# Kernel optimization log

Hardware: AMD Instinct MI355X
Metric: run time of the kernel (lower is better)

## Reference

```python
import jax, jax.numpy as jnp
import numpy as np
import math

N, T, V, C = 64, 256, 25, 64  # batch, frames, joints, channels (in==out)
D = C  # out_channels
EPS = 1e-5


def _shift_indices(v, c):
    i = np.arange(v)[:, None]
    j = np.arange(c)[None, :]
    shift_in = ((i * c + j + j * c) % (c * v)).reshape(-1)
    shift_out = ((i * c + j - j * c) % (c * v)).reshape(-1)
    return shift_in.astype(np.int64), shift_out.astype(np.int64)


def setup_inputs() -> dict:
    key = jax.random.key(0)
    k1, k2 = jax.random.split(key)
    si, so = _shift_indices(V, D)
    return {
        "x0": jax.random.normal(k1, (N, T, V, C), dtype=jnp.float32),
        "Linear_weight": jax.random.normal(k2, (C, D), dtype=jnp.float32) * math.sqrt(1.0 / D),
        "Linear_bias": jnp.zeros((1, 1, D), dtype=jnp.float32),
        "Feature_Mask": jnp.zeros((1, V, C), dtype=jnp.float32),
        "gamma": jnp.ones((V * D,), dtype=jnp.float32),
        "beta": jnp.zeros((V * D,), dtype=jnp.float32),
        "shift_in": jnp.asarray(si),
        "shift_out": jnp.asarray(so),
    }


def reference(x0, Linear_weight, Linear_bias, Feature_Mask, gamma, beta, shift_in, shift_out):
    n, t, v, c = x0.shape
    d = Linear_weight.shape[1]
    # shift-in gather over flattened (node, channel) axis
    x = x0.reshape(n * t, v * c)[:, shift_in].reshape(n * t, v, c)
    # learned feature mask (tanh + 1)
    x = x * (jnp.tanh(Feature_Mask) + 1.0)
    # pointwise channel transform + bias
    x = jnp.einsum('nwc,cd->nwd', x, Linear_weight) + Linear_bias
    # shift-out gather
    x = x.reshape(n * t, v * d)[:, shift_out]
    # BatchNorm1d (training mode): batch stats over n*t rows, biased var
    mean = jnp.mean(x, axis=0)
    var = jnp.var(x, axis=0)
    x = (x - mean) * (gamma / jnp.sqrt(var + EPS)) + beta
    # residual (in_channels == out_channels -> identity down) + ReLU
    y = jax.nn.relu(x.reshape(n, t, v, d) + x0)
    # original returns (n, out_channels, t, v)
    return jnp.transpose(y, (0, 3, 1, 2))
```

## Files before the change

### kernel.cpp

```cpp
#include <hip/hip_runtime.h>
#include <math.h>


typedef __attribute__((ext_vector_type(8))) short bf16x8;
typedef __attribute__((ext_vector_type(4))) float f32x4;

__device__ __forceinline__ ushort f2bf(float f) {
  uint u; __builtin_memcpy(&u, &f, 4);
  u += 0x7fffu + ((u >> 16) & 1u);
  return (ushort)(u >> 16);
}
__device__ __forceinline__ float bf2f(ushort b) {
  uint u = ((uint)b) << 16; float f; __builtin_memcpy(&f, &u, 4); return f;
}

__global__ void k_prep(const float* __restrict__ mask, float* __restrict__ ws) {
  int i = blockIdx.x * 256 + threadIdx.x;
  if (i < 1600) {
    int w = i >> 6, c = i & 63;
    int wr = (w + c) % 25;
    ((ushort*)ws)[wr * 64 + c] = f2bf(tanhf(mask[i]) + 1.0f);
  }
  for (int j = 8000 + i; j < 8000 + 64 * 3200; j += gridDim.x * 256)
    ws[j] = 0.0f;
}

__global__ void k_finalize(const float* __restrict__ gamma,
                           const float* __restrict__ beta,
                           float* __restrict__ ws) {
  int q = blockIdx.x * 256 + threadIdx.x;
  if (q >= 1600) return;
  float sum = 0.f, sq = 0.f;
  #pragma unroll 4
  for (int s = 0; s < 64; ++s) {
    sum += ws[8000 + s * 3200 + q];
    sq  += ws[8000 + s * 3200 + 1600 + q];
  }
  const float inv = 1.0f / 16384.0f;
  float mean = sum * inv;
  float var  = sq * inv - mean * mean;
  float istd = rsqrtf(var + 1e-5f);
  int w = q >> 6, d = q & 63;
  int p = ((w + d) % 25) * 64 + d;
  float mul = gamma[p] * istd;
  ws[4800 + q] = mul;
  ws[6400 + q] = beta[p] - mean * mul;
}

template<int PASS>
__launch_bounds__(256, 4)
__global__ void k_main(const float* __restrict__ x0,
                       const float* __restrict__ Wg,
                       float* ws,
                       float* __restrict__ out) {
  __shared__ __align__(8)  ushort s_maskm[1600];
  __shared__ __align__(16) ushort s_A[4096];
  __shared__ float s_raw[PASS == 2 ? 3400 : 4];
  __shared__ float s_aux[3200];

  const int tid = threadIdx.x;
  const int lr  = tid & 63;
  const int wid = tid >> 6;

  for (int i = tid; i < 800; i += 256)
    ((uint*)s_maskm)[i] = ((const uint*)ws)[i];
  for (int i = tid; i < 2048; i += 256)
    ((uint*)s_A)[i] = 0u;

  bf16x8 wfrag[2][4];
  #pragma unroll
  for (int ks = 0; ks < 2; ++ks)
    #pragma unroll
    for (int nt = 0; nt < 4; ++nt) {
      const int d = nt * 16 + (lr & 15);
      const int cb = ks * 32 + (lr >> 4) * 8;
      #pragma unroll
      for (int j = 0; j < 8; ++j)
        wfrag[ks][nt][j] = (short)f2bf(Wg[(cb + j) * 64 + d]);
    }

  float cmul[16], cadd[16];
  float ssum[16], ssq[16];
  #pragma unroll
  for (int k = 0; k < 16; ++k) { ssum[k] = 0.f; ssq[k] = 0.f; }
  if constexpr (PASS == 2) {
    #pragma unroll
    for (int nt = 0; nt < 4; ++nt)
      #pragma unroll
      for (int r = 0; r < 4; ++r) {
        int row = wid * 16 + (lr >> 4) * 4 + r;
        int w = row & 31;
        int d = nt * 16 + (lr & 15);
        int qq = (w < 25) ? (w * 64 + d) : 0;
        cmul[nt * 4 + r] = ws[4800 + qq];
        cadd[nt * 4 + r] = ws[6400 + qq];
      }
  }

  const int row_base = blockIdx.x * 16;
  const int n  = row_base >> 8;
  const int t0 = row_base & 255;

  if constexpr (PASS == 1) {
    for (int i = tid; i < 3200; i += 256) s_aux[i] = 0.f;
  }
  __syncthreads();

  float4 cur0, cur1, cur2, cur3, nxt0, nxt1, nxt2, nxt3;
  {
    const float4* p = (const float4*)(x0 + (size_t)row_base * 1600);
    cur0 = p[tid]; cur1 = p[tid + 256]; cur2 = p[tid + 512];
    if (tid < 32) cur3 = p[tid + 768];
  }

  for (int rp = 0; rp < 16; rp += 2) {
    #pragma unroll
    for (int s = 0; s < 4; ++s) {
      if (s == 3 && tid >= 32) break;
      int i4 = (s < 3) ? (tid + s * 256) : (768 + tid);
      float4 v = (s == 0) ? cur0 : (s == 1) ? cur1 : (s == 2) ? cur2 : cur3;
      int r2 = (i4 >= 400) ? 1 : 0;
      int p4 = (i4 - r2 * 400) * 4;
      int wr = p4 >> 6, c0 = p4 & 63;
      if constexpr (PASS == 2)
        *(float4*)&s_raw[r2 * 1700 + wr * 68 + c0] = v;
      uint2 mm = *(const uint2*)&s_maskm[p4];
      float va[4] = {v.x, v.y, v.z, v.w};
      float ma[4] = {bf2f((ushort)(mm.x & 0xffff)), bf2f((ushort)(mm.x >> 16)),
                     bf2f((ushort)(mm.y & 0xffff)), bf2f((ushort)(mm.y >> 16))};
      int wbase = wr + 100 - c0;
      #pragma unroll
      for (int j = 0; j < 4; ++j) {
        int w = (wbase - j) % 25;
        int row = r2 * 32 + w;
        int byte = (row * 128 + (c0 + j) * 2) ^ ((w & 7) << 4);
        *(ushort*)((char*)s_A + byte) = f2bf(va[j] * ma[j]);
      }
    }

    if (rp + 2 < 16) {
      const float4* p = (const float4*)(x0 + (size_t)(row_base + rp + 2) * 1600);
      nxt0 = p[tid]; nxt1 = p[tid + 256]; nxt2 = p[tid + 512];
      if (tid < 32) nxt3 = p[tid + 768];
    }
    __syncthreads();

    const int arow = wid * 16 + (lr & 15);
    bf16x8 afrag[2];
    #pragma unroll
    for (int ks = 0; ks < 2; ++ks) {
      int byte = (arow * 128 + ks * 64 + (lr >> 4) * 16) ^ ((arow & 7) << 4);
      afrag[ks] = *(const bf16x8*)((const char*)s_A + byte);
    }
    f32x4 acc[4];
    #pragma unroll
    for (int nt = 0; nt < 4; ++nt) {
      acc[nt] = (f32x4){0.f, 0.f, 0.f, 0.f};
      #pragma unroll
      for (int ks = 0; ks < 2; ++ks)
        acc[nt] = __builtin_amdgcn_mfma_f32_16x16x32_bf16(afrag[ks], wfrag[ks][nt], acc[nt], 0, 0, 0);
    }

    if constexpr (PASS == 1) {
      #pragma unroll
      for (int nt = 0; nt < 4; ++nt)
        #pragma unroll
        for (int r = 0; r < 4; ++r) {
          float y = acc[nt][r];
          ssum[nt * 4 + r] += y;
          ssq [nt * 4 + r]  = fmaf(y, y, ssq[nt * 4 + r]);
        }
      __syncthreads();
    } else {
      #pragma unroll
      for (int nt = 0; nt < 4; ++nt)
        #pragma unroll
        for (int r = 0; r < 4; ++r) {
          int row = wid * 16 + (lr >> 4) * 4 + r;
          int r2 = row >> 5;
          int w  = row & 31;
          if (w < 25) {
            int d  = nt * 16 + (lr & 15);
            int wp = (w + d) % 25;
            float y = fmaf(acc[nt][r], cmul[nt * 4 + r], cadd[nt * 4 + r]);
            y += s_raw[r2 * 1700 + wp * 68 + d];
            s_aux[d * 50 + r2 * 25 + wp] = fmaxf(y, 0.f);
          }
        }
      __syncthreads();
      const size_t obase = (size_t)n * 409600 + (size_t)(t0 + rp) * 25;
      for (int i = tid; i < 3200; i += 256) {
        int d   = i / 50;
        int rem = i - d * 50;
        int r2  = rem / 25;
        int wp  = rem - r2 * 25;
        out[obase + (size_t)d * 6400 + r2 * 25 + wp] = s_aux[i];
      }
      __syncthreads();
    }

    if (rp + 2 < 16) {
      cur0 = nxt0; cur1 = nxt1; cur2 = nxt2;
      if (tid < 32) cur3 = nxt3;
    }
  }

  if constexpr (PASS == 1) {
    #pragma unroll
    for (int nt = 0; nt < 4; ++nt)
      #pragma unroll
      for (int r = 0; r < 4; ++r) {
        int row = wid * 16 + (lr >> 4) * 4 + r;
        int w = row & 31;
        if (w < 25) {
          int q = w * 64 + nt * 16 + (lr & 15);
          atomicAdd(&s_aux[q],        ssum[nt * 4 + r]);
          atomicAdd(&s_aux[1600 + q], ssq [nt * 4 + r]);
        }
      }
    __syncthreads();
    float* rep = ws + 8000 + (blockIdx.x & 63) * 3200;
    for (int i = tid; i < 3200; i += 256)
      atomicAdd(&rep[i], s_aux[i]);
  }
}

extern "C" void kernel_launch(void* const* d_in, const int* in_sizes, int n_in,
                              void* d_out, int out_size, void* d_ws, size_t ws_size,
                              hipStream_t stream) {
  const float* x0    = (const float*)d_in[0];
  const float* W     = (const float*)d_in[1];
  const float* mask  = (const float*)d_in[3];
  const float* gamma = (const float*)d_in[4];
  const float* beta  = (const float*)d_in[5];
  float* ws  = (float*)d_ws;
  float* out = (float*)d_out;

  k_prep    <<<200,  256, 0, stream>>>(mask, ws);
  k_main<1> <<<1024, 256, 0, stream>>>(x0, W, ws, out);
  k_finalize<<<7,    256, 0, stream>>>(gamma, beta, ws);
  k_main<2> <<<1024, 256, 0, stream>>>(x0, W, ws, out);
}
```

Before: 368.5 us.

## Materialize GEMM output to workspace and split epilogue into separate transpose kernel

When the workspace is large enough, a new path runs the mask-scaled GEMM once and writes the un-normalized outputs to the workspace. It stores per-block partial statistics in slots, reduces them in a separate kernel, then a tiled epilogue kernel reads y and x0 back to apply BN, the residual and ReLU, and writes the transposed output with float4 stores. This avoids recomputing the GEMM in a second pass and the scalar strided output stores, but adds an extra write and read of a 100MB intermediate. The fallback path also loses its register prefetch of the next x0 rows.

```diff
diff --git a/kernel.cpp b/kernel.cpp
--- a/kernel.cpp
+++ b/kernel.cpp
@@ -14,7 +14,213 @@
   uint u = ((uint)b) << 16; float f; __builtin_memcpy(&f, &u, 4); return f;
 }
 
-__global__ void k_prep(const float* __restrict__ mask, float* __restrict__ ws) {
+#define YOFF    0u
+#define SLOTOFF 26214400u
+#define SUMOFF  32768000u
+#define PRMOFF  32771200u
+#define WS_NEED ((size_t)(32771200u + 3200u) * 4u)
+
+__global__ __launch_bounds__(256, 5)
+void k_gemm(const float* __restrict__ x0, const float* __restrict__ Wg,
+            const float* __restrict__ FM, float* __restrict__ ws) {
+  __shared__ ushort s_maskm[1600];
+  __shared__ float  s_u[3200];
+  ushort* s_A = (ushort*)s_u;
+
+  const int tid = threadIdx.x;
+  const int lr  = tid & 63;
+  const int wid = tid >> 6;
+
+  for (int i = tid; i < 1600; i += 256) {
+    int w = i >> 6, c = i & 63;
+    int wr = (w + c) % 25;
+    s_maskm[wr * 64 + c] = f2bf(tanhf(FM[i]) + 1.0f);
+  }
+  for (int i = tid; i < 2048; i += 256) ((uint*)s_A)[i] = 0u;
+
+  bf16x8 wfrag[2][4];
+  #pragma unroll
+  for (int ks = 0; ks < 2; ++ks)
+    #pragma unroll
+    for (int nt = 0; nt < 4; ++nt) {
+      const int d = nt * 16 + (lr & 15);
+      const int cb = ks * 32 + (lr >> 4) * 8;
+      #pragma unroll
+      for (int j = 0; j < 8; ++j)
+        wfrag[ks][nt][j] = (short)f2bf(Wg[(cb + j) * 64 + d]);
+    }
+
+  float ssum[16], ssq[16];
+  #pragma unroll
+  for (int k = 0; k < 16; ++k) { ssum[k] = 0.f; ssq[k] = 0.f; }
+
+  const int row_base = blockIdx.x * 8;
+  __syncthreads();
+
+  for (int rp = 0; rp < 8; rp += 2) {
+    const float* xrow = x0 + (size_t)(row_base + rp) * 1600;
+    for (int i4 = tid; i4 < 800; i4 += 256) {
+      float4 v = ((const float4*)xrow)[i4];
+      int r2 = (i4 >= 400) ? 1 : 0;
+      int p4 = (i4 - r2 * 400) * 4;
+      int wr = p4 >> 6, c0 = p4 & 63;
+      uint2 mm = *(const uint2*)&s_maskm[p4];
+      float va[4] = {v.x, v.y, v.z, v.w};
+      float ma[4] = {bf2f((ushort)(mm.x & 0xffff)), bf2f((ushort)(mm.x >> 16)),
+                     bf2f((ushort)(mm.y & 0xffff)), bf2f((ushort)(mm.y >> 16))};
+      int w = (wr + 100 - c0) % 25;
+      #pragma unroll
+      for (int j = 0; j < 4; ++j) {
+        int row = r2 * 32 + w;
+        int byte = (row * 128 + (c0 + j) * 2) ^ ((w & 7) << 4);
+        *(ushort*)((char*)s_A + byte) = f2bf(va[j] * ma[j]);
+        w = (w == 0) ? 24 : (w - 1);
+      }
+    }
+    __syncthreads();
+
+    const int arow = wid * 16 + (lr & 15);
+    bf16x8 afrag[2];
+    #pragma unroll
+    for (int ks = 0; ks < 2; ++ks) {
+      int byte = (arow * 128 + ks * 64 + (lr >> 4) * 16) ^ ((arow & 7) << 4);
+      afrag[ks] = *(const bf16x8*)((const char*)s_A + byte);
+    }
+    f32x4 acc[4];
+    #pragma unroll
+    for (int nt = 0; nt < 4; ++nt) {
+      acc[nt] = (f32x4){0.f, 0.f, 0.f, 0.f};
+      #pragma unroll
+      for (int ks = 0; ks < 2; ++ks)
+        acc[nt] = __builtin_amdgcn_mfma_f32_16x16x32_bf16(afrag[ks], wfrag[ks][nt], acc[nt], 0, 0, 0);
+    }
+
+    #pragma unroll
+    for (int nt = 0; nt < 4; ++nt)
+      #pragma unroll
+      for (int r = 0; r < 4; ++r) {
+        float y = acc[nt][r];
+        ssum[nt * 4 + r] += y;
+        ssq [nt * 4 + r]  = fmaf(y, y, ssq[nt * 4 + r]);
+        int mrow = wid * 16 + (lr >> 4) * 4 + r;
+        int r2 = mrow >> 5, w = mrow & 31;
+        if (w < 25)
+          ws[YOFF + (size_t)(row_base + rp + r2) * 1600 + w * 64 + nt * 16 + (lr & 15)] = y;
+      }
+    __syncthreads();
+  }
+
+  #pragma unroll
+  for (int nt = 0; nt < 4; ++nt)
+    #pragma unroll
+    for (int r = 0; r < 4; ++r) {
+      int mrow = wid * 16 + (lr >> 4) * 4 + r;
+      int w = mrow & 31;
+      if (mrow < 32 && w < 25) {
+        int q = w * 64 + nt * 16 + (lr & 15);
+        s_u[q]        = ssum[nt * 4 + r];
+        s_u[1600 + q] = ssq [nt * 4 + r];
+      }
+    }
+  __syncthreads();
+  #pragma unroll
+  for (int nt = 0; nt < 4; ++nt)
+    #pragma unroll
+    for (int r = 0; r < 4; ++r) {
+      int mrow = wid * 16 + (lr >> 4) * 4 + r;
+      int w = mrow & 31;
+      if (mrow >= 32 && w < 25) {
+        int q = w * 64 + nt * 16 + (lr & 15);
+        s_u[q]        += ssum[nt * 4 + r];
+        s_u[1600 + q] += ssq [nt * 4 + r];
+      }
+    }
+  __syncthreads();
+  for (int i = tid; i < 3200; i += 256)
+    ws[SLOTOFF + (size_t)blockIdx.x * 3200 + i] = s_u[i];
+}
+
+__global__ void k_reduce(float* __restrict__ ws) {
+  int gid = blockIdx.x * 256 + threadIdx.x;
+  int q  = gid % 3200;
+  int sc = gid / 3200;
+  size_t base = SLOTOFF + (size_t)sc * 256 * 3200 + q;
+  float s = 0.f;
+  #pragma unroll 8
+  for (int k = 0; k < 256; ++k)
+    s += ws[base + (size_t)k * 3200];
+  atomicAdd(&ws[SUMOFF + q], s);
+}
+
+__global__ void k_params(const float* __restrict__ gamma,
+                         const float* __restrict__ beta,
+                         float* __restrict__ ws) {
+  int p = blockIdx.x * 256 + threadIdx.x;
+  if (p >= 1600) return;
+  int u = p >> 6, d = p & 63;
+  int w = (u + 75 - d) % 25;
+  int q = w * 64 + d;
+  const float inv = 1.0f / 16384.0f;
+  float mean = ws[SUMOFF + q] * inv;
+  float var  = ws[SUMOFF + 1600 + q] * inv - mean * mean;
+  float istd = rsqrtf(var + 1e-5f);
+  float mul = gamma[p] * istd;
+  ws[PRMOFF + p]        = mul;
+  ws[PRMOFF + 1600 + p] = beta[p] - mean * mul;
+}
+
+__global__ __launch_bounds__(256, 2)
+void k_epi(const float* __restrict__ x0, const float* __restrict__ ws,
+           float* __restrict__ out) {
+  __shared__ float yt[16 * 25 * 17];
+  __shared__ float xt[16 * 25 * 17];
+  __shared__ float pm[2][25 * 17];
+
+  const int tid = threadIdx.x;
+  const int n  = blockIdx.x >> 4;
+  const int t0 = (blockIdx.x & 15) * 16;
+  const size_t base_in = ((size_t)n * 256 + t0) * 1600;
+  const size_t base_out = (size_t)n * 409600 + (size_t)t0 * 25;
+
+  for (int dq = 0; dq < 4; ++dq) {
+    const int dbase = dq * 16;
+    for (int i4 = tid; i4 < 1600; i4 += 256) {
+      int t = i4 / 100, rem = i4 % 100;
+      int w = rem >> 2, f4 = rem & 3;
+      size_t g = base_in + (size_t)t * 1600 + w * 64 + dbase + f4 * 4;
+      float4 vy = *(const float4*)&ws[YOFF + g];
+      float4 vx = *(const float4*)&x0[g];
+      *(float4*)&yt[(t * 25 + w) * 17 + f4 * 4] = vy;
+      *(float4*)&xt[(t * 25 + w) * 17 + f4 * 4] = vx;
+    }
+    for (int i = tid; i < 400; i += 256) {
+      int u = i >> 4, dd = i & 15;
+      pm[0][u * 17 + dd] = ws[PRMOFF + u * 64 + dbase + dd];
+      pm[1][u * 17 + dd] = ws[PRMOFF + 1600 + u * 64 + dbase + dd];
+    }
+    __syncthreads();
+
+    for (int i4 = tid; i4 < 1600; i4 += 256) {
+      int dl = i4 / 100;
+      int d  = dbase + dl;
+      int p4 = (i4 % 100) * 4;
+      float4 o;
+      #pragma unroll
+      for (int e = 0; e < 4; ++e) {
+        int p = p4 + e;
+        int t = p / 25, u = p - t * 25;
+        int w = (u + 75 - d) % 25;
+        float val = fmaf(yt[(t * 25 + w) * 17 + dl], pm[0][u * 17 + dl],
+                         pm[1][u * 17 + dl]) + xt[(t * 25 + u) * 17 + dl];
+        o[e] = fmaxf(val, 0.f);
+      }
+      *(float4*)&out[base_out + (size_t)d * 6400 + p4] = o;
+    }
+    __syncthreads();
+  }
+}
+
+__global__ void k_prep_f(const float* __restrict__ mask, float* __restrict__ ws) {
   int i = blockIdx.x * 256 + threadIdx.x;
   if (i < 1600) {
     int w = i >> 6, c = i & 63;
@@ -25,9 +231,9 @@
     ws[j] = 0.0f;
 }
 
-__global__ void k_finalize(const float* __restrict__ gamma,
-                           const float* __restrict__ beta,
-                           float* __restrict__ ws) {
+__global__ void k_finalize_f(const float* __restrict__ gamma,
+                             const float* __restrict__ beta,
+                             float* __restrict__ ws) {
   int q = blockIdx.x * 256 + threadIdx.x;
   if (q >= 1600) return;
   float sum = 0.f, sq = 0.f;
@@ -49,10 +255,10 @@
 
 template<int PASS>
 __launch_bounds__(256, 4)
-__global__ void k_main(const float* __restrict__ x0,
-                       const float* __restrict__ Wg,
-                       float* ws,
-                       float* __restrict__ out) {
+__global__ void k_main_f(const float* __restrict__ x0,
+                         const float* __restrict__ Wg,
+                         float* ws,
+                         float* __restrict__ out) {
   __shared__ __align__(8)  ushort s_maskm[1600];
   __shared__ __align__(16) ushort s_A[4096];
   __shared__ float s_raw[PASS == 2 ? 3400 : 4];
@@ -106,19 +312,10 @@
   }
   __syncthreads();
 
-  float4 cur0, cur1, cur2, cur3, nxt0, nxt1, nxt2, nxt3;
-  {
-    const float4* p = (const float4*)(x0 + (size_t)row_base * 1600);
-    cur0 = p[tid]; cur1 = p[tid + 256]; cur2 = p[tid + 512];
-    if (tid < 32) cur3 = p[tid + 768];
-  }
-
   for (int rp = 0; rp < 16; rp += 2) {
-    #pragma unroll
-    for (int s = 0; s < 4; ++s) {
-      if (s == 3 && tid >= 32) break;
-      int i4 = (s < 3) ? (tid + s * 256) : (768 + tid);
-      float4 v = (s == 0) ? cur0 : (s == 1) ? cur1 : (s == 2) ? cur2 : cur3;
+    const float* xrow = x0 + (size_t)(row_base + rp) * 1600;
+    for (int i4 = tid; i4 < 800; i4 += 256) {
+      float4 v = ((const float4*)xrow)[i4];
       int r2 = (i4 >= 400) ? 1 : 0;
       int p4 = (i4 - r2 * 400) * 4;
       int wr = p4 >> 6, c0 = p4 & 63;
@@ -136,12 +333,6 @@
         int byte = (row * 128 + (c0 + j) * 2) ^ ((w & 7) << 4);
         *(ushort*)((char*)s_A + byte) = f2bf(va[j] * ma[j]);
       }
-    }
-
-    if (rp + 2 < 16) {
-      const float4* p = (const float4*)(x0 + (size_t)(row_base + rp + 2) * 1600);
-      nxt0 = p[tid]; nxt1 = p[tid + 256]; nxt2 = p[tid + 512];
-      if (tid < 32) nxt3 = p[tid + 768];
     }
     __syncthreads();
 
@@ -198,11 +389,6 @@
       }
       __syncthreads();
     }
-
-    if (rp + 2 < 16) {
-      cur0 = nxt0; cur1 = nxt1; cur2 = nxt2;
-      if (tid < 32) cur3 = nxt3;
-    }
   }
 
   if constexpr (PASS == 1) {
@@ -236,8 +422,16 @@
   float* ws  = (float*)d_ws;
   float* out = (float*)d_out;
 
-  k_prep    <<<200,  256, 0, stream>>>(mask, ws);
-  k_main<1> <<<1024, 256, 0, stream>>>(x0, W, ws, out);
-  k_finalize<<<7,    256, 0, stream>>>(gamma, beta, ws);
-  k_main<2> <<<1024, 256, 0, stream>>>(x0, W, ws, out);
-}
+  if (ws_size >= WS_NEED) {
+    hipMemsetAsync(ws + SUMOFF, 0, 3200 * sizeof(float), stream);
+    k_gemm  <<<2048, 256, 0, stream>>>(x0, W, mask, ws);
+    k_reduce<<<100,  256, 0, stream>>>(ws);
+    k_params<<<7,    256, 0, stream>>>(gamma, beta, ws);
+    k_epi   <<<1024, 256, 0, stream>>>(x0, ws, out);
+  } else {
+    k_prep_f    <<<200,  256, 0, stream>>>(mask, ws);
+    k_main_f<1> <<<1024, 256, 0, stream>>>(x0, W, ws, out);
+    k_finalize_f<<<7,    256, 0, stream>>>(gamma, beta, ws);
+    k_main_f<2> <<<1024, 256, 0, stream>>>(x0, W, ws, out);
+  }
+}
```

After: 364.2 us. About the same (-1.2%).
